# Optimization experiments

Hardware: AMD Instinct MI355X
Metric: run time of the kernel (lower is better)

The kernel has to match this reference:

```python
import jax, jax.numpy as jnp
import numpy as np

PATCH = 32
NUM_HEADS = 8
LN_EPS = 1e-6


def _window_starts(size, step, d):
    # replicates local_partition's loop: for i in range(0, size + step - d, step)
    starts = []
    for i in range(0, size + step - d, step):
        starts.append(min(i, size - d))
    return np.asarray(starts, dtype=np.int64)


def _window_index_grids(h, w, dh, dw, step):
    rs = _window_starts(h, step, dh)  # (nr,)
    cs = _window_starts(w, step, dw)  # (nc,)
    nr, nc = len(rs), len(cs)
    ri = rs[:, None] + np.arange(dh)  # (nr, dh)
    ci = cs[:, None] + np.arange(dw)  # (nc, dw)
    RI = np.broadcast_to(ri[:, None, :, None], (nr, nc, dh, dw)).reshape(nr * nc, dh, dw)
    CI = np.broadcast_to(ci[None, :, None, :], (nr, nc, dh, dw)).reshape(nr * nc, dh, dw)
    return RI, CI


def setup_inputs() -> dict:
    key = jax.random.key(0)
    ks = jax.random.split(key, 6)
    b, t, h, w, c = 1, 2, 48, 48, 256
    x = jax.random.normal(ks[0], (b, t, h, w, c), dtype=jnp.float32)
    scale = 0.02
    Wq = jax.random.normal(ks[1], (c, c), dtype=jnp.float32) * scale
    Wk = jax.random.normal(ks[2], (c, c), dtype=jnp.float32) * scale
    Wv = jax.random.normal(ks[3], (c, c), dtype=jnp.float32) * scale
    Wo = jax.random.normal(ks[4], (c, c), dtype=jnp.float32) * scale
    bo = jnp.zeros((c,), dtype=jnp.float32)
    ln_w = jnp.ones((c,), dtype=jnp.float32)
    ln_b = jnp.zeros((c,), dtype=jnp.float32)
    return {"x": x, "ln_w": ln_w, "ln_b": ln_b, "Wq": Wq, "Wk": Wk,
            "Wv": Wv, "Wo": Wo, "bo": bo}


def reference(x, ln_w, ln_b, Wq, Wk, Wv, Wo, bo):
    b, t, h, w, c = x.shape
    dh = dw = PATCH
    step = dh - dh // 4  # 24 for patch_size=32
    RI, CI = _window_index_grids(h, w, dh, dw, step)  # (n, dh, dw) each, static
    n = RI.shape[0]

    # LayerNorm (eps=1e-6)
    mu = jnp.mean(x, axis=-1, keepdims=True)
    var = jnp.mean((x - mu) ** 2, axis=-1, keepdims=True)
    xn = (x - mu) / jnp.sqrt(var + LN_EPS) * ln_w + ln_b

    # projections (torch Linear: y = x @ W.T), no bias for q/k/v
    q = xn @ Wq.T
    k = xn @ Wk.T
    v = xn @ Wv.T

    def partition(z):
        # z: (b, t, h, w, C) -> (b, n, t, dh, dw, C) via static gather
        zz = z[:, :, RI, CI, :]            # (b, t, n, dh, dw, C)
        return zz.transpose(0, 2, 1, 3, 4, 5)

    lq, lk, lv = partition(q), partition(k), partition(v)

    C = q.shape[-1]
    hd = C // NUM_HEADS
    S = t * dh * dw  # tokens per local window

    def to_heads(z):
        # (b, n, t, dh, dw, C) -> (b*n, heads, S, hd)
        return z.reshape(b * n, S, NUM_HEADS, hd).transpose(0, 2, 1, 3)

    Q, K, V = to_heads(lq), to_heads(lk), to_heads(lv)

    scores = jnp.einsum('bhqd,bhkd->bhqk', Q, K) * (hd ** -0.5)
    attn = jax.nn.softmax(scores, axis=-1)
    out = jnp.einsum('bhqk,bhkd->bhqd', attn, V)  # (b*n, heads, S, hd)

    # back to (b, t, n, dh, dw, C)
    out = out.transpose(0, 2, 1, 3).reshape(b, n, t, dh, dw, C)
    out = out.transpose(0, 2, 1, 3, 4, 5)

    # local_reverse: overlap-add then average by coverage count
    acc = jnp.zeros((b, t, h, w, C), dtype=x.dtype)
    acc = acc.at[:, :, RI, CI, :].add(out)
    cnt = jnp.zeros((h, w), dtype=x.dtype).at[RI, CI].add(1.0)
    merged = acc / cnt[None, None, :, :, None]

    return merged @ Wo.T + bo
```

## Files before the change

### kernel.cpp

```cpp
#include <hip/hip_runtime.h>
#include <hip/hip_bf16.h>

#define TT 2
#define HH 48
#define WW 48
#define CC 256
#define NHEADS 8
#define HDIM 32
#define SEQ 2048
#define NPIX (TT*HH*WW)
#define NPC  (NPIX*CC)
#define MFIX 12.0f
#define LSZ  (4*NHEADS*SEQ)
#define OFS  (4*SEQ*CC)
#define SPLITS 4

typedef __attribute__((ext_vector_type(8))) short bf16x8;
typedef __attribute__((ext_vector_type(4))) short bf16x4;
typedef __attribute__((ext_vector_type(4))) float f32x4;

#if __has_builtin(__builtin_amdgcn_exp2f)
#define EXP2(x) __builtin_amdgcn_exp2f(x)
#else
#define EXP2(x) exp2f(x)
#endif
#if __has_builtin(__builtin_amdgcn_rcpf)
#define RCP(x) __builtin_amdgcn_rcpf(x)
#else
#define RCP(x) (1.0f/(x))
#endif

__device__ inline unsigned cvt_pk_bf16(float lo, float hi) {
    unsigned r;
    asm("v_cvt_pk_bf16_f32 %0, %1, %2" : "=v"(r) : "v"(lo), "v"(hi));
    return r;
}
__device__ inline f32x4 mfma16(bf16x4 a, bf16x4 b, f32x4 c) {
    asm("v_mfma_f32_16x16x16_bf16 %0, %1, %2, %0" : "+v"(c) : "v"(a), "v"(b));
    return c;
}
__device__ inline f32x4 b2f4(bf16x4 v) {
    union { bf16x4 b; unsigned short u[4]; } t; t.b = v;
    f32x4 r;
    #pragma unroll
    for (int i = 0; i < 4; ++i) { union { unsigned u; float f; } c; c.u = ((unsigned)t.u[i]) << 16; r[i] = c.f; }
    return r;
}

__global__ __launch_bounds__(256) void k_prep(
    const float* __restrict__ Wq, const float* __restrict__ Wk,
    const float* __restrict__ Wv, const float* __restrict__ Wo,
    __hip_bfloat16* __restrict__ wfp, __hip_bfloat16* __restrict__ wofp)
{
    const float QSC = 0.17677669529663688f * 1.4426950408889634f;
    const int idx = blockIdx.x * 256 + threadIdx.x;
    const int e = idx * 4;
    const int grow = e >> 8;
    const int c = e & 255;
    const float* src;
    float sc = 1.f;
    if (grow < 256)      { src = Wq + e;          sc = QSC; }
    else if (grow < 512) { src = Wk + (e - 65536); }
    else if (grow < 768) { src = Wv + (e - 131072); }
    else                 { src = Wo + (e - 196608); }
    const float4 t = *reinterpret_cast<const float4*>(src);
    uint2 st;
    st.x = cvt_pk_bf16(t.x * sc, t.y * sc);
    st.y = cvt_pk_bf16(t.z * sc, t.w * sc);
    const int r8  = grow & 255;
    const int oct = r8 >> 4, m16 = r8 & 15;
    const int k   = c >> 5, g = (c >> 3) & 3, j0 = c & 7;
    if (grow < 768) {
        const int mat = grow >> 8;
        const size_t o = ((size_t)((mat * 16 + oct) * 8 + k) * 64 + g * 16 + m16) * 8 + j0;
        *reinterpret_cast<uint2*>(wfp + o) = st;
    } else {
        const size_t o = ((size_t)(oct * 8 + k) * 64 + g * 16 + m16) * 8 + j0;
        *reinterpret_cast<uint2*>(wofp + o) = st;
    }
}

__global__ __launch_bounds__(256) void k_ln(
    const float* __restrict__ x,
    const float* __restrict__ lnw, const float* __restrict__ lnb,
    __hip_bfloat16* __restrict__ xnb)
{
    const int lane = threadIdx.x & 63;
    const int pix  = blockIdx.x * 4 + (threadIdx.x >> 6);
    const float4 xv = *reinterpret_cast<const float4*>(x + (size_t)pix * CC + lane * 4);
    float s  = xv.x + xv.y + xv.z + xv.w;
    float s2 = xv.x*xv.x + xv.y*xv.y + xv.z*xv.z + xv.w*xv.w;
    #pragma unroll
    for (int m = 1; m < 64; m <<= 1) {
        s  += __shfl_xor(s,  m, 64);
        s2 += __shfl_xor(s2, m, 64);
    }
    const float mu   = s * (1.0f / CC);
    const float var  = s2 * (1.0f / CC) - mu * mu;
    const float rstd = rsqrtf(var + 1e-6f);
    const float4 w4 = *reinterpret_cast<const float4*>(lnw + lane * 4);
    const float4 b4 = *reinterpret_cast<const float4*>(lnb + lane * 4);
    uint2 st;
    st.x = cvt_pk_bf16((xv.x - mu) * rstd * w4.x + b4.x, (xv.y - mu) * rstd * w4.y + b4.y);
    st.y = cvt_pk_bf16((xv.z - mu) * rstd * w4.z + b4.z, (xv.w - mu) * rstd * w4.w + b4.w);
    *reinterpret_cast<uint2*>(xnb + (size_t)pix * CC + lane * 4) = st;
}

__global__ __launch_bounds__(256) void k_qkv(
    const __hip_bfloat16* __restrict__ xnb,
    const __hip_bfloat16* __restrict__ wfp,
    __hip_bfloat16* __restrict__ qb, __hip_bfloat16* __restrict__ kb,
    __hip_bfloat16* __restrict__ vtb)
{
    const int tid  = threadIdx.x;
    const int wv_  = tid >> 6;
    const int lane = tid & 63;
    const int mat  = blockIdx.x / 144;
    const int r    = blockIdx.x % 144;
    const int p0   = (r >> 1) * 64;
    const int ocg  = r & 1;
    const int m16 = lane & 15, g = lane >> 4;
    const int pxb = p0 + wv_ * 16;

    bf16x8 xf[8];
    #pragma unroll
    for (int k = 0; k < 8; ++k)
        xf[k] = *reinterpret_cast<const bf16x8*>(
            xnb + (size_t)(pxb + m16) * CC + k * 32 + g * 8);

    for (int o8 = 0; o8 < 8; ++o8) {
        const int oct = ocg * 8 + o8;
        const __hip_bfloat16* wt = wfp + ((size_t)(mat * 16 + oct) * 8) * 512;
        f32x4 c = {0.f, 0.f, 0.f, 0.f};
        if (mat < 2) {
            #pragma unroll
            for (int k = 0; k < 8; ++k) {
                const bf16x8 wf = *reinterpret_cast<const bf16x8*>(wt + (size_t)k * 512 + lane * 8);
                c = __builtin_amdgcn_mfma_f32_16x16x32_bf16(wf, xf[k], c, 0, 0, 0);
            }
            uint2 st;
            st.x = cvt_pk_bf16(c[0], c[1]);
            st.y = cvt_pk_bf16(c[2], c[3]);
            __hip_bfloat16* dst = (mat == 0) ? qb : kb;
            *reinterpret_cast<uint2*>(dst + (size_t)(pxb + m16) * CC + oct * 16 + g * 4) = st;
        } else {
            #pragma unroll
            for (int k = 0; k < 8; ++k) {
                const bf16x8 wf = *reinterpret_cast<const bf16x8*>(wt + (size_t)k * 512 + lane * 8);
                c = __builtin_amdgcn_mfma_f32_16x16x32_bf16(xf[k], wf, c, 0, 0, 0);
            }
            uint2 st;
            st.x = cvt_pk_bf16(c[0], c[1]);
            st.y = cvt_pk_bf16(c[2], c[3]);
            *reinterpret_cast<uint2*>(vtb + (size_t)(oct * 16 + m16) * NPIX + pxb + g * 4) = st;
        }
    }
}

__global__ __launch_bounds__(512, 4) void k_attn(
    const __hip_bfloat16* __restrict__ qb, const __hip_bfloat16* __restrict__ kb,
    const __hip_bfloat16* __restrict__ vtb, __hip_bfloat16* __restrict__ Opm,
    float* __restrict__ lsb)
{
    __shared__ __hip_bfloat16 lds[32768];
    const int tid  = threadIdx.x;
    const int lane = tid & 63;
    const int wsub = tid >> 6;
    const int bid  = blockIdx.x;
    const int grp  = bid & 127;
    const int qq   = bid >> 7;
    const int split = grp >> 5;
    const int wh    = grp & 31;
    const int win   = wh >> 3;
    const int head  = wh & 7;
    const int rs = (win >> 1) * 16, cs = (win & 1) * 16;
    const int tt = split >> 1;
    const int y0 = (split & 1) * 16;
    const int rowbase = (tt * HH + rs) * WW + cs;
    const int qblk64 = qq * 8 + wsub;
    const int g = lane >> 4, q16 = lane & 15;

    {
        const int k16 = tid & 15, gk = (tid >> 4) & 3;
        #pragma unroll
        for (int pass = 0; pass < 4; ++pass) {
            const int slot = pass * 512 + tid;
            const int T = slot >> 6;
            const int key = T * 16 + k16;
            const int pix = rowbase + (y0 + (key >> 5)) * WW + (key & 31);
            *reinterpret_cast<bf16x8*>(&lds[(size_t)slot * 8]) =
                *reinterpret_cast<const bf16x8*>(kb + (size_t)pix * CC + head * HDIM + gk * 8);
        }
        const int cch = tid >> 4, s16 = tid & 15;
        const int dtc = cch >> 4, qvc = cch & 15;
        const __hip_bfloat16* vrow = vtb + (size_t)(head * HDIM + cch) * NPIX;
        #pragma unroll
        for (int i = 0; i < 4; ++i) {
            const int key0 = i * 128 + s16 * 8;
            const int pix0 = rowbase + (y0 + (key0 >> 5)) * WW + (key0 & 31);
            union { bf16x8 v; bf16x4 h[2]; } u;
            u.v = *reinterpret_cast<const bf16x8*>(vrow + pix0);
            const int T2  = key0 >> 4;
            const int gv0 = (key0 & 15) >> 2;
            #pragma unroll
            for (int h = 0; h < 2; ++h) {
                const int slot = ((T2 * 2 + dtc) * 4 + gv0 + h) * 16 + qvc;
                *reinterpret_cast<bf16x4*>(&lds[16384 + (size_t)slot * 4]) = u.h[h];
            }
        }
    }

    bf16x8 qf[4];
    #pragma unroll
    for (int qt = 0; qt < 4; ++qt) {
        const int s = qblk64 * 64 + qt * 16 + q16;
        const int pix = ((s >> 10) * HH + rs + ((s >> 5) & 31)) * WW + cs + (s & 31);
        qf[qt] = *reinterpret_cast<const bf16x8*>(qb + (size_t)pix * CC + head * HDIM + g * 8);
    }

    f32x4 acc[2][4];
    #pragma unroll
    for (int a = 0; a < 2; ++a)
        #pragma unroll
        for (int b = 0; b < 4; ++b) acc[a][b] = (f32x4){0.f, 0.f, 0.f, 0.f};
    float lsum[4] = {0.f, 0.f, 0.f, 0.f};

    __syncthreads();

    const bf16x8* kvec = reinterpret_cast<const bf16x8*>(&lds[0]);
    const bf16x4* vvec = reinterpret_cast<const bf16x4*>(&lds[16384]);

    for (int it = 0; it < 16; ++it) {
        const bf16x8 kf0 = kvec[it * 128 + lane];
        const bf16x8 kf1 = kvec[it * 128 + 64 + lane];
        const bf16x4 vf00 = vvec[it * 256 + lane];
        const bf16x4 vf10 = vvec[it * 256 + 64 + lane];
        const bf16x4 vf01 = vvec[it * 256 + 128 + lane];
        const bf16x4 vf11 = vvec[it * 256 + 192 + lane];
        #pragma unroll
        for (int qt = 0; qt < 4; ++qt) {
            const f32x4 z = {0.f, 0.f, 0.f, 0.f};
            const f32x4 s0 = __builtin_amdgcn_mfma_f32_16x16x32_bf16(kf0, qf[qt], z, 0, 0, 0);
            const f32x4 s1 = __builtin_amdgcn_mfma_f32_16x16x32_bf16(kf1, qf[qt], z, 0, 0, 0);
            const float p00 = EXP2(s0[0] - MFIX), p01 = EXP2(s0[1] - MFIX);
            const float p02 = EXP2(s0[2] - MFIX), p03 = EXP2(s0[3] - MFIX);
            const float p10 = EXP2(s1[0] - MFIX), p11 = EXP2(s1[1] - MFIX);
            const float p12 = EXP2(s1[2] - MFIX), p13 = EXP2(s1[3] - MFIX);
            lsum[qt] += ((p00 + p01) + (p02 + p03)) + ((p10 + p11) + (p12 + p13));
            union { unsigned u[2]; bf16x4 v; } pA, pB;
            pA.u[0] = cvt_pk_bf16(p00, p01); pA.u[1] = cvt_pk_bf16(p02, p03);
            pB.u[0] = cvt_pk_bf16(p10, p11); pB.u[1] = cvt_pk_bf16(p12, p13);
            acc[0][qt] = mfma16(vf00, pA.v, acc[0][qt]);
            acc[1][qt] = mfma16(vf10, pA.v, acc[1][qt]);
            acc[0][qt] = mfma16(vf01, pB.v, acc[0][qt]);
            acc[1][qt] = mfma16(vf11, pB.v, acc[1][qt]);
        }
    }

    float* lp = lsb + (size_t)split * LSZ + (size_t)wh * SEQ;
    __hip_bfloat16* Osp = Opm + (size_t)split * OFS + (size_t)win * SEQ * CC + head * HDIM;
    #pragma unroll
    for (int qt = 0; qt < 4; ++qt) {
        float l = lsum[qt];
        l += __shfl_xor(l, 16, 64);
        l += __shfl_xor(l, 32, 64);
        const int s = qblk64 * 64 + qt * 16 + q16;
        if (g == 0) lp[s] = l;
        #pragma unroll
        for (int dt = 0; dt < 2; ++dt) {
            uint2 st;
            st.x = cvt_pk_bf16(acc[dt][qt][0], acc[dt][qt][1]);
            st.y = cvt_pk_bf16(acc[dt][qt][2], acc[dt][qt][3]);
            *reinterpret_cast<uint2*>(Osp + (size_t)s * CC + dt * 16 + g * 4) = st;
        }
    }
}

__global__ __launch_bounds__(256) void k_mproj(
    const __hip_bfloat16* __restrict__ Opm, const float* __restrict__ lsb,
    const __hip_bfloat16* __restrict__ wofp, const float* __restrict__ bo,
    float* __restrict__ out)
{
    __shared__ __hip_bfloat16 md[16][264];
    const int tid  = threadIdx.x;
    const int wv_  = tid >> 6;
    const int L    = tid & 63;
    const int head = L >> 3;
    const int p0   = blockIdx.x * 16;

    for (int i = 0; i < 4; ++i) {
        const int pl = wv_ * 4 + i;
        const int p  = p0 + pl;
        const int tt  = p / (HH * WW);
        const int rem = p % (HH * WW);
        const int y   = rem / WW;
        const int xc  = rem % WW;
        f32x4 a = {0.f, 0.f, 0.f, 0.f};
        int cnt = 0;
        for (int wr = 0; wr < 2; ++wr) {
            const int ii = y - wr * 16;
            if (ii < 0 || ii >= 32) continue;
            for (int wc = 0; wc < 2; ++wc) {
                const int jj = xc - wc * 16;
                if (jj < 0 || jj >= 32) continue;
                const int win = wr * 2 + wc;
                const int srow = tt * 1024 + ii * 32 + jj;
                const size_t ob = ((size_t)win * SEQ + srow) * CC + L * 4;
                const size_t li = (size_t)(win * NHEADS + head) * SEQ + srow;
                f32x4 acc4 = {0.f, 0.f, 0.f, 0.f};
                float l = 0.f;
                #pragma unroll
                for (int sp = 0; sp < SPLITS; ++sp) {
                    acc4 += b2f4(*reinterpret_cast<const bf16x4*>(Opm + (size_t)sp * OFS + ob));
                    l += lsb[(size_t)sp * LSZ + li];
                }
                a += acc4 * RCP(l);
                ++cnt;
            }
        }
        const float ic = (cnt == 1) ? 1.0f : ((cnt == 2) ? 0.5f : 0.25f);
        uint2 st;
        st.x = cvt_pk_bf16(a[0] * ic, a[1] * ic);
        st.y = cvt_pk_bf16(a[2] * ic, a[3] * ic);
        *reinterpret_cast<uint2*>(&md[pl][L * 4]) = st;
    }
    __syncthreads();

    const int m16 = L & 15, g = L >> 4;
    bf16x8 xf[8];
    #pragma unroll
    for (int k = 0; k < 8; ++k)
        xf[k] = *reinterpret_cast<const bf16x8*>(&md[m16][k * 32 + g * 8]);

    #pragma unroll
    for (int oct = 0; oct < 4; ++oct) {
        const int octG = wv_ * 4 + oct;
        const int ocb  = octG * 16;
        const __hip_bfloat16* wt = wofp + (size_t)octG * 8 * 512;
        f32x4 c = {0.f, 0.f, 0.f, 0.f};
        #pragma unroll
        for (int k = 0; k < 8; ++k) {
            const bf16x8 wf = *reinterpret_cast<const bf16x8*>(wt + (size_t)k * 512 + L * 8);
            c = __builtin_amdgcn_mfma_f32_16x16x32_bf16(wf, xf[k], c, 0, 0, 0);
        }
        const float4 b4 = *reinterpret_cast<const float4*>(bo + ocb + g * 4);
        c[0] += b4.x; c[1] += b4.y; c[2] += b4.z; c[3] += b4.w;
        *reinterpret_cast<f32x4*>(out + (size_t)(p0 + m16) * CC + ocb + g * 4) = c;
    }
}

extern "C" void kernel_launch(void* const* d_in, const int* in_sizes, int n_in,
                              void* d_out, int out_size, void* d_ws, size_t ws_size,
                              hipStream_t stream)
{
    const float* x   = (const float*)d_in[0];
    const float* lnw = (const float*)d_in[1];
    const float* lnb = (const float*)d_in[2];
    const float* Wq  = (const float*)d_in[3];
    const float* Wk  = (const float*)d_in[4];
    const float* Wv  = (const float*)d_in[5];
    const float* Wo  = (const float*)d_in[6];
    const float* bo  = (const float*)d_in[7];

    __hip_bfloat16* qb   = (__hip_bfloat16*)d_ws;
    __hip_bfloat16* kb   = qb + NPC;
    __hip_bfloat16* vtb  = kb + NPC;
    __hip_bfloat16* xnb  = vtb + NPC;
    __hip_bfloat16* Opm  = xnb + NPC;
    __hip_bfloat16* wfp  = Opm + (size_t)SPLITS * OFS;
    __hip_bfloat16* wofp = wfp + 196608;
    float* lsb = (float*)(wofp + 65536);

    k_prep<<<256, 256, 0, stream>>>(Wq, Wk, Wv, Wo, wfp, wofp);
    k_ln<<<NPIX / 4, 256, 0, stream>>>(x, lnw, lnb, xnb);
    k_qkv<<<432, 256, 0, stream>>>(xnb, wfp, qb, kb, vtb);
    k_attn<<<512, 512, 0, stream>>>(qb, kb, vtb, Opm, lsb);
    k_mproj<<<288, 256, 0, stream>>>(Opm, lsb, wofp, bo, (float*)d_out);
}
```

Baseline: 71.25 us.

## Merge weight prep with LayerNorm, split QKV grid finer, compute row sums via MFMA

Weight conversion and LayerNorm now run as one launch using a block-index split, which removes a kernel launch. The QKV projection grid doubles, with each block handling four output octets instead of eight, to raise occupancy. In attention, the per-row softmax denominator comes from an extra MFMA against a ones vector instead of scalar adds plus shuffles. This shifts work from VALU onto the matrix unit, but the sums are now accumulated from bf16-rounded probabilities.

```diff
diff --git a/kernel.cpp b/kernel.cpp
--- a/kernel.cpp
+++ b/kernel.cpp
@@ -47,63 +47,63 @@
     return r;
 }
 
-__global__ __launch_bounds__(256) void k_prep(
+__global__ __launch_bounds__(256) void k_pre(
     const float* __restrict__ Wq, const float* __restrict__ Wk,
     const float* __restrict__ Wv, const float* __restrict__ Wo,
-    __hip_bfloat16* __restrict__ wfp, __hip_bfloat16* __restrict__ wofp)
-{
-    const float QSC = 0.17677669529663688f * 1.4426950408889634f;
-    const int idx = blockIdx.x * 256 + threadIdx.x;
-    const int e = idx * 4;
-    const int grow = e >> 8;
-    const int c = e & 255;
-    const float* src;
-    float sc = 1.f;
-    if (grow < 256)      { src = Wq + e;          sc = QSC; }
-    else if (grow < 512) { src = Wk + (e - 65536); }
-    else if (grow < 768) { src = Wv + (e - 131072); }
-    else                 { src = Wo + (e - 196608); }
-    const float4 t = *reinterpret_cast<const float4*>(src);
-    uint2 st;
-    st.x = cvt_pk_bf16(t.x * sc, t.y * sc);
-    st.y = cvt_pk_bf16(t.z * sc, t.w * sc);
-    const int r8  = grow & 255;
-    const int oct = r8 >> 4, m16 = r8 & 15;
-    const int k   = c >> 5, g = (c >> 3) & 3, j0 = c & 7;
-    if (grow < 768) {
-        const int mat = grow >> 8;
-        const size_t o = ((size_t)((mat * 16 + oct) * 8 + k) * 64 + g * 16 + m16) * 8 + j0;
-        *reinterpret_cast<uint2*>(wfp + o) = st;
-    } else {
-        const size_t o = ((size_t)(oct * 8 + k) * 64 + g * 16 + m16) * 8 + j0;
-        *reinterpret_cast<uint2*>(wofp + o) = st;
-    }
-}
-
-__global__ __launch_bounds__(256) void k_ln(
     const float* __restrict__ x,
     const float* __restrict__ lnw, const float* __restrict__ lnb,
+    __hip_bfloat16* __restrict__ wfp, __hip_bfloat16* __restrict__ wofp,
     __hip_bfloat16* __restrict__ xnb)
 {
-    const int lane = threadIdx.x & 63;
-    const int pix  = blockIdx.x * 4 + (threadIdx.x >> 6);
-    const float4 xv = *reinterpret_cast<const float4*>(x + (size_t)pix * CC + lane * 4);
-    float s  = xv.x + xv.y + xv.z + xv.w;
-    float s2 = xv.x*xv.x + xv.y*xv.y + xv.z*xv.z + xv.w*xv.w;
-    #pragma unroll
-    for (int m = 1; m < 64; m <<= 1) {
-        s  += __shfl_xor(s,  m, 64);
-        s2 += __shfl_xor(s2, m, 64);
-    }
-    const float mu   = s * (1.0f / CC);
-    const float var  = s2 * (1.0f / CC) - mu * mu;
-    const float rstd = rsqrtf(var + 1e-6f);
-    const float4 w4 = *reinterpret_cast<const float4*>(lnw + lane * 4);
-    const float4 b4 = *reinterpret_cast<const float4*>(lnb + lane * 4);
-    uint2 st;
-    st.x = cvt_pk_bf16((xv.x - mu) * rstd * w4.x + b4.x, (xv.y - mu) * rstd * w4.y + b4.y);
-    st.y = cvt_pk_bf16((xv.z - mu) * rstd * w4.z + b4.z, (xv.w - mu) * rstd * w4.w + b4.w);
-    *reinterpret_cast<uint2*>(xnb + (size_t)pix * CC + lane * 4) = st;
+    const int tid = threadIdx.x;
+    if (blockIdx.x < 256) {
+        const float QSC = 0.17677669529663688f * 1.4426950408889634f;
+        const int idx = blockIdx.x * 256 + tid;
+        const int e = idx * 4;
+        const int grow = e >> 8;
+        const int c = e & 255;
+        const float* src;
+        float sc = 1.f;
+        if (grow < 256)      { src = Wq + e;          sc = QSC; }
+        else if (grow < 512) { src = Wk + (e - 65536); }
+        else if (grow < 768) { src = Wv + (e - 131072); }
+        else                 { src = Wo + (e - 196608); }
+        const float4 t = *reinterpret_cast<const float4*>(src);
+        uint2 st;
+        st.x = cvt_pk_bf16(t.x * sc, t.y * sc);
+        st.y = cvt_pk_bf16(t.z * sc, t.w * sc);
+        const int r8  = grow & 255;
+        const int oct = r8 >> 4, m16 = r8 & 15;
+        const int k   = c >> 5, g = (c >> 3) & 3, j0 = c & 7;
+        if (grow < 768) {
+            const int mat = grow >> 8;
+            const size_t o = ((size_t)((mat * 16 + oct) * 8 + k) * 64 + g * 16 + m16) * 8 + j0;
+            *reinterpret_cast<uint2*>(wfp + o) = st;
+        } else {
+            const size_t o = ((size_t)(oct * 8 + k) * 64 + g * 16 + m16) * 8 + j0;
+            *reinterpret_cast<uint2*>(wofp + o) = st;
+        }
+    } else {
+        const int lane = tid & 63;
+        const int pix  = (blockIdx.x - 256) * 4 + (tid >> 6);
+        const float4 xv = *reinterpret_cast<const float4*>(x + (size_t)pix * CC + lane * 4);
+        float s  = xv.x + xv.y + xv.z + xv.w;
+        float s2 = xv.x*xv.x + xv.y*xv.y + xv.z*xv.z + xv.w*xv.w;
+        #pragma unroll
+        for (int m = 1; m < 64; m <<= 1) {
+            s  += __shfl_xor(s,  m, 64);
+            s2 += __shfl_xor(s2, m, 64);
+        }
+        const float mu   = s * (1.0f / CC);
+        const float var  = s2 * (1.0f / CC) - mu * mu;
+        const float rstd = rsqrtf(var + 1e-6f);
+        const float4 w4 = *reinterpret_cast<const float4*>(lnw + lane * 4);
+        const float4 b4 = *reinterpret_cast<const float4*>(lnb + lane * 4);
+        uint2 st;
+        st.x = cvt_pk_bf16((xv.x - mu) * rstd * w4.x + b4.x, (xv.y - mu) * rstd * w4.y + b4.y);
+        st.y = cvt_pk_bf16((xv.z - mu) * rstd * w4.z + b4.z, (xv.w - mu) * rstd * w4.w + b4.w);
+        *reinterpret_cast<uint2*>(xnb + (size_t)pix * CC + lane * 4) = st;
+    }
 }
 
 __global__ __launch_bounds__(256) void k_qkv(
@@ -115,10 +115,10 @@
     const int tid  = threadIdx.x;
     const int wv_  = tid >> 6;
     const int lane = tid & 63;
-    const int mat  = blockIdx.x / 144;
-    const int r    = blockIdx.x % 144;
-    const int p0   = (r >> 1) * 64;
-    const int ocg  = r & 1;
+    const int mat  = blockIdx.x / 288;
+    const int r    = blockIdx.x % 288;
+    const int p0   = (r >> 2) * 64;
+    const int ocg  = r & 3;
     const int m16 = lane & 15, g = lane >> 4;
     const int pxb = p0 + wv_ * 16;
 
@@ -128,8 +128,9 @@
         xf[k] = *reinterpret_cast<const bf16x8*>(
             xnb + (size_t)(pxb + m16) * CC + k * 32 + g * 8);
 
-    for (int o8 = 0; o8 < 8; ++o8) {
-        const int oct = ocg * 8 + o8;
+    #pragma unroll
+    for (int o4 = 0; o4 < 4; ++o4) {
+        const int oct = ocg * 4 + o4;
         const __hip_bfloat16* wt = wfp + ((size_t)(mat * 16 + oct) * 8) * 512;
         f32x4 c = {0.f, 0.f, 0.f, 0.f};
         if (mat < 2) {
@@ -219,11 +220,15 @@
     }
 
     f32x4 acc[2][4];
-    #pragma unroll
-    for (int a = 0; a < 2; ++a)
-        #pragma unroll
-        for (int b = 0; b < 4; ++b) acc[a][b] = (f32x4){0.f, 0.f, 0.f, 0.f};
-    float lsum[4] = {0.f, 0.f, 0.f, 0.f};
+    f32x4 accl[4];
+    #pragma unroll
+    for (int b = 0; b < 4; ++b) {
+        acc[0][b] = (f32x4){0.f, 0.f, 0.f, 0.f};
+        acc[1][b] = (f32x4){0.f, 0.f, 0.f, 0.f};
+        accl[b]   = (f32x4){0.f, 0.f, 0.f, 0.f};
+    }
+    const short one_bf = (short)0x3F80;
+    const bf16x4 vones = {one_bf, one_bf, one_bf, one_bf};
 
     __syncthreads();
 
@@ -246,14 +251,15 @@
             const float p02 = EXP2(s0[2] - MFIX), p03 = EXP2(s0[3] - MFIX);
             const float p10 = EXP2(s1[0] - MFIX), p11 = EXP2(s1[1] - MFIX);
             const float p12 = EXP2(s1[2] - MFIX), p13 = EXP2(s1[3] - MFIX);
-            lsum[qt] += ((p00 + p01) + (p02 + p03)) + ((p10 + p11) + (p12 + p13));
             union { unsigned u[2]; bf16x4 v; } pA, pB;
             pA.u[0] = cvt_pk_bf16(p00, p01); pA.u[1] = cvt_pk_bf16(p02, p03);
             pB.u[0] = cvt_pk_bf16(p10, p11); pB.u[1] = cvt_pk_bf16(p12, p13);
             acc[0][qt] = mfma16(vf00, pA.v, acc[0][qt]);
             acc[1][qt] = mfma16(vf10, pA.v, acc[1][qt]);
+            accl[qt]   = mfma16(vones, pA.v, accl[qt]);
             acc[0][qt] = mfma16(vf01, pB.v, acc[0][qt]);
             acc[1][qt] = mfma16(vf11, pB.v, acc[1][qt]);
+            accl[qt]   = mfma16(vones, pB.v, accl[qt]);
         }
     }
 
@@ -261,9 +267,7 @@
     __hip_bfloat16* Osp = Opm + (size_t)split * OFS + (size_t)win * SEQ * CC + head * HDIM;
     #pragma unroll
     for (int qt = 0; qt < 4; ++qt) {
-        float l = lsum[qt];
-        l += __shfl_xor(l, 16, 64);
-        l += __shfl_xor(l, 32, 64);
+        const float l = accl[qt][0];
         const int s = qblk64 * 64 + qt * 16 + q16;
         if (g == 0) lp[s] = l;
         #pragma unroll
@@ -371,9 +375,8 @@
     __hip_bfloat16* wofp = wfp + 196608;
     float* lsb = (float*)(wofp + 65536);
 
-    k_prep<<<256, 256, 0, stream>>>(Wq, Wk, Wv, Wo, wfp, wofp);
-    k_ln<<<NPIX / 4, 256, 0, stream>>>(x, lnw, lnb, xnb);
-    k_qkv<<<432, 256, 0, stream>>>(xnb, wfp, qb, kb, vtb);
+    k_pre<<<1408, 256, 0, stream>>>(Wq, Wk, Wv, Wo, x, lnw, lnb, wfp, wofp, xnb);
+    k_qkv<<<864, 256, 0, stream>>>(xnb, wfp, qb, kb, vtb);
     k_attn<<<512, 512, 0, stream>>>(qb, kb, vtb, Opm, lsb);
     k_mproj<<<288, 256, 0, stream>>>(Opm, lsb, wofp, bo, (float*)d_out);
 }
```

After: 66.98 us. 6.0% less time.
